# Optimization experiments

Hardware: AMD Instinct MI355X
Metric: run time of the kernel (lower is better)

The kernel has to match this reference:

```python
import jax, jax.numpy as jnp
import numpy as np

VOCAB = 10000
HID = 256
BATCH = 32
STEPS = 256


def setup_inputs() -> dict:
    key = jax.random.key(0)
    k1, k2, k3, k4 = jax.random.split(key, 4)
    # glorot-uniform style scaling
    s_xh = np.sqrt(6.0 / (VOCAB + HID)).astype(np.float32)
    s_hh = np.sqrt(6.0 / (HID + HID)).astype(np.float32)
    s_d = np.sqrt(6.0 / (HID + VOCAB)).astype(np.float32)
    return {
        "tokens": jax.random.randint(k1, (BATCH, STEPS), 0, VOCAB, dtype=jnp.int32),
        "W_xh": jax.random.uniform(k2, (VOCAB, HID), jnp.float32, -s_xh, s_xh),
        "W_hh": jax.random.uniform(k3, (HID, HID), jnp.float32, -s_hh, s_hh),
        "b_h": jnp.zeros((HID,), jnp.float32),
        "W_d": jax.random.uniform(k4, (HID, VOCAB), jnp.float32, -s_d, s_d),
        "b_d": jnp.zeros((VOCAB,), jnp.float32),
        "h0": jnp.zeros((BATCH, HID), jnp.float32),
    }


def reference(tokens, W_xh, W_hh, b_h, W_d, b_d, h0):
    # call(): X = one_hot(transpose(tokens), vocab)  -> time-major [T, B, V]
    # one_hot(x) @ W_xh is exactly a row gather from W_xh (same math, efficient form)
    xw = W_xh[jnp.transpose(tokens)]  # [T, B, H]

    # SimpleRNNCell: h_t = tanh(x_t @ W_xh + h_{t-1} @ W_hh + b)
    def step(h, xt):
        h_new = jnp.tanh(xt + h @ W_hh + b_h)
        return h_new, h_new

    state, Y = jax.lax.scan(step, h0, xw)  # Y: [T, B, H], state: [B, H]

    # Dense over flattened sequence outputs -> [T*B, vocab]
    output = Y.reshape(-1, Y.shape[-1]) @ W_d + b_d
    return output, state
```

## Files before the change

kernel.cpp:

```cpp
#include <hip/hip_runtime.h>
#include <hip/hip_bf16.h>

#define VOCAB 10000
#define HID 256
#define BATCH 32
#define STEPS 256
#define MROWS (STEPS * BATCH)

typedef __bf16 bf16x8 __attribute__((ext_vector_type(8)));
typedef float f32x4 __attribute__((ext_vector_type(4)));
typedef unsigned short u16x4 __attribute__((ext_vector_type(4)));

template <int CTRL>
static __device__ __forceinline__ float dpp_add(float s) {
    int t = __builtin_amdgcn_update_dpp(
        0, __builtin_bit_cast(int, s), CTRL, 0xf, 0xf, true);
    return s + __builtin_bit_cast(float, t);
}
#define DPP_XOR1 0xB1
#define DPP_XOR2 0x4E

static __device__ __forceinline__ float swz4_add(float s) {
    int t = __builtin_amdgcn_ds_swizzle(__builtin_bit_cast(int, s), 0x101F);
    return s + __builtin_bit_cast(float, t);
}

__global__ void transpose_wd_kernel(const float* __restrict__ Wd,
                                    __hip_bfloat16* __restrict__ WdT) {
    __shared__ __hip_bfloat16 tile[64][68];
    const int n0 = blockIdx.x * 64;
    const int k0 = blockIdx.y * 64;
    const int tid = threadIdx.x;
    const int lane = tid & 63;
    const int w = tid >> 6;

#pragma unroll
    for (int i = 0; i < 16; ++i) {
        int k = w * 16 + i;
        int n = lane;
        float v = (n0 + n < VOCAB) ? Wd[(size_t)(k0 + k) * VOCAB + n0 + n] : 0.f;
        tile[n][k] = __float2bfloat16(v);
    }
    __syncthreads();
#pragma unroll
    for (int i = 0; i < 16; ++i) {
        int n = w * 16 + i;
        int k = lane;
        if (n0 + n < VOCAB)
            WdT[(size_t)(n0 + n) * HID + k0 + k] = tile[n][k];
    }
}

__global__ void transpose_whh_kernel(const float* __restrict__ Whh,
                                     float* __restrict__ WhhT) {
    __shared__ float tile[64][65];
    const int j0 = blockIdx.x * 64;
    const int k0 = blockIdx.y * 64;
    const int tid = threadIdx.x;
    const int lane = tid & 63;
    const int w = tid >> 6;

#pragma unroll
    for (int i = 0; i < 16; ++i) {
        int k = w * 16 + i;
        tile[lane][k] = Whh[(size_t)(k0 + k) * HID + j0 + lane];
    }
    __syncthreads();
#pragma unroll
    for (int i = 0; i < 16; ++i) {
        int j = w * 16 + i;
        WhhT[(size_t)(j0 + j) * HID + k0 + lane] = tile[j][lane];
    }
}

#define HSEG 36

__global__ __launch_bounds__(512, 2)
__attribute__((amdgpu_waves_per_eu(2, 2)))
void rnn_kernel(const int* __restrict__ tokens, const float* __restrict__ Wxh,
                const float* __restrict__ WhhT, const float* __restrict__ bh,
                const float* __restrict__ h0, __hip_bfloat16* __restrict__ ybf,
                float* __restrict__ state_out) {
    const int b = blockIdx.x;
    const int tid = threadIdx.x;
    const int cg = tid >> 3;
    const int q = tid & 7;
    const int c0 = cg * 4;

    __shared__ alignas(16) float hseg[2][8][HSEG];

    float w[4][32];
#pragma unroll
    for (int c = 0; c < 4; ++c) {
        const float4* wp = reinterpret_cast<const float4*>(
            WhhT + (size_t)(c0 + c) * HID + q * 32);
#pragma unroll
        for (int i4 = 0; i4 < 8; ++i4) {
            float4 v = wp[i4];
            w[c][i4 * 4 + 0] = v.x;
            w[c][i4 * 4 + 1] = v.y;
            w[c][i4 * 4 + 2] = v.z;
            w[c][i4 * 4 + 3] = v.w;
        }
    }

    const float4 bj = *reinterpret_cast<const float4*>(&bh[c0]);
    const int* trow = tokens + b * STEPS;

    if (q == 0) {
        *reinterpret_cast<float4*>(&hseg[0][c0 >> 5][c0 & 31]) =
            *reinterpret_cast<const float4*>(&h0[b * HID + c0]);
    }

    float4 xv = *reinterpret_cast<const float4*>(&Wxh[(size_t)trow[0] * HID + c0]);
    __syncthreads();

    float hn[4] = {0.f, 0.f, 0.f, 0.f};
    int cur = 0;
    for (int t = 0; t < STEPS; ++t) {
        int ti = (t + 1 < STEPS) ? t + 1 : STEPS - 1;
        float4 xn = *reinterpret_cast<const float4*>(
            &Wxh[(size_t)trow[ti] * HID + c0]);

        const float* hb = &hseg[cur][q][0];
        float s[4] = {0.f, 0.f, 0.f, 0.f};
#pragma unroll
        for (int j4 = 0; j4 < 8; ++j4) {
            float4 hv = *reinterpret_cast<const float4*>(&hb[j4 * 4]);
#pragma unroll
            for (int c = 0; c < 4; ++c)
                s[c] += hv.x * w[c][j4 * 4 + 0] + hv.y * w[c][j4 * 4 + 1] +
                        hv.z * w[c][j4 * 4 + 2] + hv.w * w[c][j4 * 4 + 3];
        }
#pragma unroll
        for (int c = 0; c < 4; ++c) {
            s[c] = dpp_add<DPP_XOR1>(s[c]);
            s[c] = dpp_add<DPP_XOR2>(s[c]);
            s[c] = swz4_add(s[c]);
        }

        const float x4[4] = {xv.x, xv.y, xv.z, xv.w};
        const float b4[4] = {bj.x, bj.y, bj.z, bj.w};
#pragma unroll
        for (int c = 0; c < 4; ++c) {
            float z = x4[c] + b4[c] + s[c];
            float e = __expf(2.f * z);
            hn[c] = 1.f - 2.f / (e + 1.f);
        }

        if (q == 0) {
            *reinterpret_cast<float4*>(&hseg[cur ^ 1][c0 >> 5][c0 & 31]) =
                make_float4(hn[0], hn[1], hn[2], hn[3]);
        } else if (q == 1) {
            u16x4 yv;
#pragma unroll
            for (int c = 0; c < 4; ++c)
                yv[c] = __builtin_bit_cast(unsigned short,
                                           __float2bfloat16(hn[c]));
            *reinterpret_cast<u16x4*>(
                &ybf[(size_t)t * (BATCH * HID) + b * HID + c0]) = yv;
        }

        __syncthreads();
        cur ^= 1;
        xv = xn;
    }
    if (q == 2) {
        *reinterpret_cast<float4*>(&state_out[b * HID + c0]) =
            make_float4(hn[0], hn[1], hn[2], hn[3]);
    }
}

__global__ __launch_bounds__(256)
void gemm_kernel(const __hip_bfloat16* __restrict__ A,
                 const __hip_bfloat16* __restrict__ BT,
                 const float* __restrict__ bd,
                 float* __restrict__ C) {
    const int m0 = blockIdx.x * 128;
    const int n0 = blockIdx.y * 128;
    const int tid = threadIdx.x;
    const int lane = tid & 63;
    const int wv = tid >> 6;
    const int wr = wv >> 1;
    const int wc = wv & 1;
    const int r15 = lane & 15;
    const int g = lane >> 4;

    __shared__ alignas(16) __hip_bfloat16 As[128][264];

#pragma unroll
    for (int c = 0; c < 16; ++c) {
        int chunk = c * 256 + tid;
        int row = chunk >> 5;
        int cc = chunk & 31;
        bf16x8 av = *reinterpret_cast<const bf16x8*>(
            &A[(size_t)(m0 + row) * HID + cc * 8]);
        *reinterpret_cast<bf16x8*>(&As[row][cc * 8]) = av;
    }
    __syncthreads();

    const __hip_bfloat16* brow[4];
    bool bok[4];
#pragma unroll
    for (int n = 0; n < 4; ++n) {
        int rn = n0 + wc * 64 + n * 16 + r15;
        bok[n] = rn < VOCAB;
        brow[n] = BT + (size_t)(bok[n] ? rn : 0) * HID;
    }
    bf16x8 bzero;
#pragma unroll
    for (int e = 0; e < 8; ++e) bzero[e] = (__bf16)0.f;

    f32x4 acc[4][4] = {};
    bf16x8 bcur[4];
#pragma unroll
    for (int n = 0; n < 4; ++n)
        bcur[n] = bok[n] ? *reinterpret_cast<const bf16x8*>(&brow[n][g * 8])
                         : bzero;

    for (int kk8 = 0; kk8 < 8; ++kk8) {
        bf16x8 bnext[4];
        if (kk8 < 7) {
            int off = (kk8 + 1) * 32 + g * 8;
#pragma unroll
            for (int n = 0; n < 4; ++n)
                bnext[n] = bok[n]
                    ? *reinterpret_cast<const bf16x8*>(&brow[n][off])
                    : bzero;
        }
        bf16x8 af[4];
#pragma unroll
        for (int m = 0; m < 4; ++m)
            af[m] = *reinterpret_cast<const bf16x8*>(
                &As[wr * 64 + m * 16 + r15][kk8 * 32 + g * 8]);
#pragma unroll
        for (int m = 0; m < 4; ++m)
#pragma unroll
            for (int n = 0; n < 4; ++n)
                acc[m][n] = __builtin_amdgcn_mfma_f32_16x16x32_bf16(
                    bcur[n], af[m], acc[m][n], 0, 0, 0);
        if (kk8 < 7) {
#pragma unroll
            for (int n = 0; n < 4; ++n) bcur[n] = bnext[n];
        }
    }

#pragma unroll
    for (int m = 0; m < 4; ++m) {
        int row = m0 + wr * 64 + m * 16 + r15;
#pragma unroll
        for (int n = 0; n < 4; ++n) {
            int cb = n0 + wc * 64 + n * 16;
            if (cb + 15 < VOCAB) {
                int col = cb + g * 4;
                float4 bv = *reinterpret_cast<const float4*>(&bd[col]);
                f32x4 v = acc[m][n];
                v[0] += bv.x; v[1] += bv.y; v[2] += bv.z; v[3] += bv.w;
                *reinterpret_cast<f32x4*>(&C[(size_t)row * VOCAB + col]) = v;
            }
        }
    }
}

extern "C" void kernel_launch(void* const* d_in, const int* in_sizes, int n_in,
                              void* d_out, int out_size, void* d_ws, size_t ws_size,
                              hipStream_t stream) {
    const int* tokens  = (const int*)d_in[0];
    const float* Wxh   = (const float*)d_in[1];
    const float* Whh   = (const float*)d_in[2];
    const float* bh    = (const float*)d_in[3];
    const float* Wd    = (const float*)d_in[4];
    const float* bd    = (const float*)d_in[5];
    const float* h0    = (const float*)d_in[6];

    float* out = (float*)d_out;
    float* state_out = out + (size_t)MROWS * VOCAB;

    char* wsb = (char*)d_ws;
    __hip_bfloat16* ybf = (__hip_bfloat16*)wsb;
    __hip_bfloat16* wdt = (__hip_bfloat16*)(wsb + (size_t)MROWS * HID * 2);
    float* whhT = (float*)(wsb + (size_t)MROWS * HID * 2 + (size_t)VOCAB * HID * 2);

    hipLaunchKernelGGL(transpose_whh_kernel, dim3(4, 4), dim3(256), 0, stream,
                       Whh, whhT);
    hipLaunchKernelGGL(transpose_wd_kernel, dim3(157, 4), dim3(256), 0, stream,
                       Wd, wdt);
    hipLaunchKernelGGL(rnn_kernel, dim3(BATCH), dim3(512), 0, stream,
                       tokens, Wxh, whhT, bh, h0, ybf, state_out);
    hipLaunchKernelGGL(gemm_kernel, dim3(64, 79), dim3(256), 0, stream,
                       ybf, wdt, bd, out);
}
```

Before: 423.1 us.

## Split RNN recurrence across 16 lanes per column group with DPP row-shift reduction

Result: slower. 493.8 us (+16.7%).

```diff
diff --git a/kernel.cpp b/kernel.cpp
--- a/kernel.cpp
+++ b/kernel.cpp
@@ -17,13 +17,6 @@
         0, __builtin_bit_cast(int, s), CTRL, 0xf, 0xf, true);
     return s + __builtin_bit_cast(float, t);
 }
-#define DPP_XOR1 0xB1
-#define DPP_XOR2 0x4E
-
-static __device__ __forceinline__ float swz4_add(float s) {
-    int t = __builtin_amdgcn_ds_swizzle(__builtin_bit_cast(int, s), 0x101F);
-    return s + __builtin_bit_cast(float, t);
-}
 
 __global__ void transpose_wd_kernel(const float* __restrict__ Wd,
                                     __hip_bfloat16* __restrict__ WdT) {
@@ -73,85 +66,81 @@
     }
 }
 
-#define HSEG 36
-
-__global__ __launch_bounds__(512, 2)
-__attribute__((amdgpu_waves_per_eu(2, 2)))
+__global__ __attribute__((amdgpu_flat_work_group_size(1024, 1024),
+                          amdgpu_waves_per_eu(4, 4)))
 void rnn_kernel(const int* __restrict__ tokens, const float* __restrict__ Wxh,
                 const float* __restrict__ WhhT, const float* __restrict__ bh,
                 const float* __restrict__ h0, __hip_bfloat16* __restrict__ ybf,
                 float* __restrict__ state_out) {
     const int b = blockIdx.x;
     const int tid = threadIdx.x;
-    const int cg = tid >> 3;
-    const int q = tid & 7;
+    const int cg = tid >> 4;
+    const int q = tid & 15;
     const int c0 = cg * 4;
 
-    __shared__ alignas(16) float hseg[2][8][HSEG];
-
-    float w[4][32];
+    __shared__ alignas(16) float hseg[2][16][20];
+
+    f32x4 w4[4][4];
 #pragma unroll
     for (int c = 0; c < 4; ++c) {
-        const float4* wp = reinterpret_cast<const float4*>(
-            WhhT + (size_t)(c0 + c) * HID + q * 32);
-#pragma unroll
-        for (int i4 = 0; i4 < 8; ++i4) {
-            float4 v = wp[i4];
-            w[c][i4 * 4 + 0] = v.x;
-            w[c][i4 * 4 + 1] = v.y;
-            w[c][i4 * 4 + 2] = v.z;
-            w[c][i4 * 4 + 3] = v.w;
-        }
+        const f32x4* wp = reinterpret_cast<const f32x4*>(
+            WhhT + (size_t)(c0 + c) * HID + q * 16);
+#pragma unroll
+        for (int j = 0; j < 4; ++j) w4[c][j] = wp[j];
     }
 
     const float4 bj = *reinterpret_cast<const float4*>(&bh[c0]);
     const int* trow = tokens + b * STEPS;
 
-    if (q == 0) {
-        *reinterpret_cast<float4*>(&hseg[0][c0 >> 5][c0 & 31]) =
+    if (q == 15) {
+        *reinterpret_cast<float4*>(&hseg[0][c0 >> 4][c0 & 15]) =
             *reinterpret_cast<const float4*>(&h0[b * HID + c0]);
     }
 
-    float4 xv = *reinterpret_cast<const float4*>(&Wxh[(size_t)trow[0] * HID + c0]);
+    float4 xv = make_float4(0.f, 0.f, 0.f, 0.f);
+    if (q == 15)
+        xv = *reinterpret_cast<const float4*>(&Wxh[(size_t)trow[0] * HID + c0]);
     __syncthreads();
 
     float hn[4] = {0.f, 0.f, 0.f, 0.f};
     int cur = 0;
     for (int t = 0; t < STEPS; ++t) {
         int ti = (t + 1 < STEPS) ? t + 1 : STEPS - 1;
-        float4 xn = *reinterpret_cast<const float4*>(
-            &Wxh[(size_t)trow[ti] * HID + c0]);
+        float4 xn = xv;
+        if (q == 15)
+            xn = *reinterpret_cast<const float4*>(
+                &Wxh[(size_t)trow[ti] * HID + c0]);
 
         const float* hb = &hseg[cur][q][0];
         float s[4] = {0.f, 0.f, 0.f, 0.f};
 #pragma unroll
-        for (int j4 = 0; j4 < 8; ++j4) {
+        for (int j4 = 0; j4 < 4; ++j4) {
             float4 hv = *reinterpret_cast<const float4*>(&hb[j4 * 4]);
 #pragma unroll
-            for (int c = 0; c < 4; ++c)
-                s[c] += hv.x * w[c][j4 * 4 + 0] + hv.y * w[c][j4 * 4 + 1] +
-                        hv.z * w[c][j4 * 4 + 2] + hv.w * w[c][j4 * 4 + 3];
+            for (int c = 0; c < 4; ++c) {
+                s[c] += hv.x * w4[c][j4][0] + hv.y * w4[c][j4][1] +
+                        hv.z * w4[c][j4][2] + hv.w * w4[c][j4][3];
+            }
         }
 #pragma unroll
         for (int c = 0; c < 4; ++c) {
-            s[c] = dpp_add<DPP_XOR1>(s[c]);
-            s[c] = dpp_add<DPP_XOR2>(s[c]);
-            s[c] = swz4_add(s[c]);
-        }
-
-        const float x4[4] = {xv.x, xv.y, xv.z, xv.w};
-        const float b4[4] = {bj.x, bj.y, bj.z, bj.w};
-#pragma unroll
-        for (int c = 0; c < 4; ++c) {
-            float z = x4[c] + b4[c] + s[c];
-            float e = __expf(2.f * z);
-            hn[c] = 1.f - 2.f / (e + 1.f);
-        }
-
-        if (q == 0) {
-            *reinterpret_cast<float4*>(&hseg[cur ^ 1][c0 >> 5][c0 & 31]) =
+            s[c] = dpp_add<0x111>(s[c]);
+            s[c] = dpp_add<0x112>(s[c]);
+            s[c] = dpp_add<0x114>(s[c]);
+            s[c] = dpp_add<0x118>(s[c]);
+        }
+
+        if (q == 15) {
+            const float x4[4] = {xv.x, xv.y, xv.z, xv.w};
+            const float b4[4] = {bj.x, bj.y, bj.z, bj.w};
+#pragma unroll
+            for (int c = 0; c < 4; ++c) {
+                float z = x4[c] + b4[c] + s[c];
+                float e = __expf(2.f * z);
+                hn[c] = 1.f - 2.f / (e + 1.f);
+            }
+            *reinterpret_cast<float4*>(&hseg[cur ^ 1][c0 >> 4][c0 & 15]) =
                 make_float4(hn[0], hn[1], hn[2], hn[3]);
-        } else if (q == 1) {
             u16x4 yv;
 #pragma unroll
             for (int c = 0; c < 4; ++c)
@@ -165,7 +154,7 @@
         cur ^= 1;
         xv = xn;
     }
-    if (q == 2) {
+    if (q == 15) {
         *reinterpret_cast<float4*>(&state_out[b * HID + c0]) =
             make_float4(hn[0], hn[1], hn[2], hn[3]);
     }
@@ -285,7 +274,7 @@
                        Whh, whhT);
     hipLaunchKernelGGL(transpose_wd_kernel, dim3(157, 4), dim3(256), 0, stream,
                        Wd, wdt);
-    hipLaunchKernelGGL(rnn_kernel, dim3(BATCH), dim3(512), 0, stream,
+    hipLaunchKernelGGL(rnn_kernel, dim3(BATCH), dim3(1024), 0, stream,
                        tokens, Wxh, whhT, bh, h0, ybf, state_out);
     hipLaunchKernelGGL(gemm_kernel, dim3(64, 79), dim3(256), 0, stream,
                        ybf, wdt, bd, out);
```
